# Kernel optimization log

Measured on AMD Instinct MI355X. Metric: run time of the kernel, lower is better.

## Reference

```python
import jax, jax.numpy as jnp
import numpy as np

T = 64    # target_len
D = 256   # av_dim


def setup_inputs() -> dict:
    key = jax.random.key(0)
    ks = jax.random.split(key, 8)
    B, L = 128, 512
    return {
        "acoustic_seq": jax.random.normal(ks[0], (B, L, D), jnp.float32),
        "visual_seq": jax.random.normal(ks[1], (B, L, D), jnp.float32),
        "IS_BAG_list": jnp.ones((B, L), jnp.int32),
        # h_fc: Linear(target_len, target_len)
        "Wh": jax.random.normal(ks[2], (T, T), jnp.float32) * 0.05,
        "bh": jax.random.normal(ks[3], (T,), jnp.float32) * 0.05,
        # w_fc: Linear(av_dim, av_dim)
        "Ww": jax.random.normal(ks[4], (D, D), jnp.float32) * 0.05,
        "bw": jax.random.normal(ks[5], (D,), jnp.float32) * 0.05,
        # conv: Conv2d(2, 1, kernel_size=1) -> two scalars + bias
        "conv_w": jax.random.normal(ks[6], (2,), jnp.float32) * 0.5,
        "conv_b": jax.random.normal(ks[7], (1,), jnp.float32) * 0.1,
    }


def reference(acoustic_seq, visual_seq, IS_BAG_list, Wh, bh, Ww, bw, conv_w, conv_b):
    B, L, Dd = acoustic_seq.shape
    G = L // T  # uniform group size (deterministic variant of random group sizes)
    mapping = jnp.repeat(jnp.arange(T), G)  # [L] pooled-frame index per original frame

    # resize_sequence (m_len > target_len branch): group-mean pooling to T frames
    aco_p = acoustic_seq.reshape(B, T, G, Dd).mean(axis=2)  # [B,T,D]
    vis_p = visual_seq.reshape(B, T, G, Dd).mean(axis=2)    # [B,T,D]

    # c_attention = sigmoid(Conv2d(2->1, 1x1)(stack([aco,vis], ch)))
    c_att = jax.nn.sigmoid(conv_w[0] * aco_p + conv_w[1] * vis_p + conv_b[0])  # [B,T,D]

    # hw_attention = mean over channel dim
    hw = 0.5 * (aco_p + vis_p)                                 # [B,T,D]
    h_att = jax.nn.sigmoid(hw.mean(axis=2) @ Wh.T + bh)        # [B,T]
    w_att = jax.nn.sigmoid(hw.mean(axis=1) @ Ww.T + bw)        # [B,D]

    # recover_sequence (m_len > target_len): gather attention[mapping]
    h_full = h_att[:, mapping][..., None]   # [B,L,1]
    w_full = w_att[:, None, :]              # [B,1,D]
    c_full = c_att[:, mapping, :]           # [B,L,D]

    scale = (h_full + w_full + c_full) / 3.0
    mask = (IS_BAG_list == 1)[..., None]    # [B,L,1]
    aco_out = jnp.where(mask, acoustic_seq * scale, acoustic_seq)
    vis_out = jnp.where(mask, visual_seq * scale, visual_seq)
    return aco_out, vis_out
```

## Files before the change

kernel.cpp:

```cpp
#include <hip/hip_runtime.h>
#include <math.h>

#define BB 128
#define LL 512
#define DD 256
#define TT 64
#define GG 8
#define NQ (DD/4)

typedef float f32x4 __attribute__((ext_vector_type(4)));

__device__ __forceinline__ float sigm(float x) {
    return 1.0f / (1.0f + __expf(-x));
}
__device__ __forceinline__ f32x4 sigm4(f32x4 z) {
    f32x4 r;
    r.x = sigm(z.x); r.y = sigm(z.y); r.z = sigm(z.z); r.w = sigm(z.w);
    return r;
}

__global__ __launch_bounds__(256) void k_sum(
    const f32x4* __restrict__ aco4, const f32x4* __restrict__ vis4,
    float* __restrict__ rowMean,
    float* __restrict__ colpart)
{
    const int tid  = threadIdx.x;
    const int w    = tid >> 6;
    const int lane = tid & 63;
    const int bk   = blockIdx.x;
    const int b    = bk >> 3;
    const int t8   = bk & 7;

    const size_t rowBase = (size_t)b * LL + (size_t)t8 * 64 + (size_t)w * 16;

    f32x4 hw0 = 0.f, hw1 = 0.f;
#pragma unroll
    for (int j = 0; j < 8; ++j)
        hw0 += aco4[(rowBase + j) * NQ + lane] + vis4[(rowBase + j) * NQ + lane];
#pragma unroll
    for (int j = 0; j < 8; ++j)
        hw1 += aco4[(rowBase + 8 + j) * NQ + lane] + vis4[(rowBase + 8 + j) * NQ + lane];
    hw0 *= 0.0625f;
    hw1 *= 0.0625f;

    float s0 = hw0.x + hw0.y + hw0.z + hw0.w;
    float s1 = hw1.x + hw1.y + hw1.z + hw1.w;
#pragma unroll
    for (int off = 32; off > 0; off >>= 1) {
        s0 += __shfl_xor(s0, off, 64);
        s1 += __shfl_xor(s1, off, 64);
    }
    if (lane == 0) {
        const int btBase = b * TT + t8 * 8 + 2 * w;
        rowMean[btBase]     = s0 * (1.0f / DD);
        rowMean[btBase + 1] = s1 * (1.0f / DD);
    }

    __shared__ __align__(16) float red[4][DD];
    *reinterpret_cast<f32x4*>(&red[w][lane * 4]) = hw0 + hw1;
    __syncthreads();
    colpart[(size_t)bk * DD + tid] =
        red[0][tid] + red[1][tid] + red[2][tid] + red[3][tid];
}

__global__ __launch_bounds__(256) void k_gates(
    const float* __restrict__ colpart, const float* __restrict__ rowMean,
    const float* __restrict__ Wh, const float* __restrict__ bh,
    const float* __restrict__ Ww, const float* __restrict__ bw,
    float* __restrict__ h_att, float* __restrict__ w_att)
{
    const int b = blockIdx.x;
    const int d = threadIdx.x;

    __shared__ float rm[TT];
    __shared__ float cm[DD];

    {
        float cs = 0.f;
#pragma unroll
        for (int p = 0; p < 8; ++p)
            cs += colpart[(size_t)(b * 8 + p) * DD + d];
        cm[d] = cs * (1.0f / TT);
        if (d < TT) rm[d] = rowMean[b * TT + d];
    }
    __syncthreads();

    if (d < TT) {
        float acc = bh[d];
#pragma unroll 8
        for (int j = 0; j < TT; ++j) acc += rm[j] * Wh[d * TT + j];
        h_att[b * TT + d] = sigm(acc);
    }
    {
        float acc = bw[d];
        const f32x4* Wr = reinterpret_cast<const f32x4*>(Ww + (size_t)d * DD);
#pragma unroll 8
        for (int kq = 0; kq < NQ; ++kq) {
            f32x4 wq = Wr[kq];
            acc += cm[4 * kq] * wq.x + cm[4 * kq + 1] * wq.y +
                   cm[4 * kq + 2] * wq.z + cm[4 * kq + 3] * wq.w;
        }
        w_att[b * DD + d] = sigm(acc);
    }
}

__global__ __launch_bounds__(256) void k_apply(
    const f32x4* __restrict__ aco4, const f32x4* __restrict__ vis4,
    const int* __restrict__ isb,
    const float* __restrict__ h_att, const float* __restrict__ w_att,
    const float* __restrict__ cw, const float* __restrict__ cb,
    f32x4* __restrict__ out4)
{
    const int tid = threadIdx.x;
    const int sub = tid >> 6;
    const int q   = tid & 63;
    const int bk  = blockIdx.x;
    const int b   = bk >> 4;
    const int t   = (bk & 15) * 4 + sub;

    const size_t rowBase = (size_t)b * LL + (size_t)t * GG;
    const size_t N4      = (size_t)BB * LL * NQ;

    f32x4 A[8], V[8];
#pragma unroll
    for (int j = 0; j < 8; ++j) A[j] = aco4[(rowBase + j) * NQ + q];
#pragma unroll
    for (int j = 0; j < 8; ++j) V[j] = vis4[(rowBase + j) * NQ + q];

    f32x4 pa = A[0] + A[1] + A[2] + A[3] + A[4] + A[5] + A[6] + A[7];
    f32x4 pv = V[0] + V[1] + V[2] + V[3] + V[4] + V[5] + V[6] + V[7];
    pa *= 0.125f;
    pv *= 0.125f;

    const f32x4 c  = sigm4(cw[0] * pa + cw[1] * pv + cb[0]);
    const float h  = h_att[b * TT + t];
    const f32x4 w4 = *reinterpret_cast<const f32x4*>(w_att + (size_t)b * DD + q * 4);
    const f32x4 sc = (h + w4 + c) * (1.0f / 3.0f);

#pragma unroll
    for (int j = 0; j < 8; ++j) {
        const size_t ridx = rowBase + j;
        const size_t idx  = ridx * NQ + q;
        const int m = isb[ridx];
        f32x4 a = A[j];
        f32x4 v = V[j];
        if (m == 1) { a *= sc; v *= sc; }
        __builtin_nontemporal_store(a, &out4[idx]);
        __builtin_nontemporal_store(v, &out4[N4 + idx]);
    }
}

extern "C" void kernel_launch(void* const* d_in, const int* in_sizes, int n_in,
                              void* d_out, int out_size, void* d_ws, size_t ws_size,
                              hipStream_t stream) {
    const f32x4* aco = (const f32x4*)d_in[0];
    const f32x4* vis = (const f32x4*)d_in[1];
    const int*   isb = (const int*)d_in[2];
    const float* Wh  = (const float*)d_in[3];
    const float* bh  = (const float*)d_in[4];
    const float* Ww  = (const float*)d_in[5];
    const float* bw  = (const float*)d_in[6];
    const float* cw  = (const float*)d_in[7];
    const float* cb  = (const float*)d_in[8];
    f32x4* out = (f32x4*)d_out;

    float* ws = (float*)d_ws;
    float* rowMean = ws;
    float* colpart = rowMean + BB * TT;
    float* h_att   = colpart + 1024 * DD;
    float* w_att   = h_att + BB * TT;

    k_sum<<<1024, 256, 0, stream>>>(aco, vis, rowMean, colpart);
    k_gates<<<BB, 256, 0, stream>>>(colpart, rowMean, Wh, bh, Ww, bw, h_att, w_att);
    k_apply<<<2048, 256, 0, stream>>>(aco, vis, isb, h_att, w_att, cw, cb, out);
}
```

Before: 77.21 us.

## Fuse gate computation into apply kernel, recomputing gates per block

```diff
diff --git a/kernel.cpp b/kernel.cpp
--- a/kernel.cpp
+++ b/kernel.cpp
@@ -63,51 +63,12 @@
         red[0][tid] + red[1][tid] + red[2][tid] + red[3][tid];
 }
 
-__global__ __launch_bounds__(256) void k_gates(
+__global__ __launch_bounds__(256) void k_apply(
+    const f32x4* __restrict__ aco4, const f32x4* __restrict__ vis4,
+    const int* __restrict__ isb,
     const float* __restrict__ colpart, const float* __restrict__ rowMean,
     const float* __restrict__ Wh, const float* __restrict__ bh,
     const float* __restrict__ Ww, const float* __restrict__ bw,
-    float* __restrict__ h_att, float* __restrict__ w_att)
-{
-    const int b = blockIdx.x;
-    const int d = threadIdx.x;
-
-    __shared__ float rm[TT];
-    __shared__ float cm[DD];
-
-    {
-        float cs = 0.f;
-#pragma unroll
-        for (int p = 0; p < 8; ++p)
-            cs += colpart[(size_t)(b * 8 + p) * DD + d];
-        cm[d] = cs * (1.0f / TT);
-        if (d < TT) rm[d] = rowMean[b * TT + d];
-    }
-    __syncthreads();
-
-    if (d < TT) {
-        float acc = bh[d];
-#pragma unroll 8
-        for (int j = 0; j < TT; ++j) acc += rm[j] * Wh[d * TT + j];
-        h_att[b * TT + d] = sigm(acc);
-    }
-    {
-        float acc = bw[d];
-        const f32x4* Wr = reinterpret_cast<const f32x4*>(Ww + (size_t)d * DD);
-#pragma unroll 8
-        for (int kq = 0; kq < NQ; ++kq) {
-            f32x4 wq = Wr[kq];
-            acc += cm[4 * kq] * wq.x + cm[4 * kq + 1] * wq.y +
-                   cm[4 * kq + 2] * wq.z + cm[4 * kq + 3] * wq.w;
-        }
-        w_att[b * DD + d] = sigm(acc);
-    }
-}
-
-__global__ __launch_bounds__(256) void k_apply(
-    const f32x4* __restrict__ aco4, const f32x4* __restrict__ vis4,
-    const int* __restrict__ isb,
-    const float* __restrict__ h_att, const float* __restrict__ w_att,
     const float* __restrict__ cw, const float* __restrict__ cb,
     f32x4* __restrict__ out4)
 {
@@ -127,14 +88,49 @@
 #pragma unroll
     for (int j = 0; j < 8; ++j) V[j] = vis4[(rowBase + j) * NQ + q];
 
+    __shared__ __align__(16) float cm[DD];
+    __shared__ __align__(16) float w_l[DD];
+    __shared__ float rm[TT];
+    __shared__ float h_l[4];
+
+    {
+        float cs = 0.f;
+#pragma unroll
+        for (int p = 0; p < 8; ++p)
+            cs += colpart[(size_t)(b * 8 + p) * DD + tid];
+        cm[tid] = cs * (1.0f / TT);
+        if (tid < TT) rm[tid] = rowMean[b * TT + tid];
+    }
+    __syncthreads();
+
+    if (tid < 4) {
+        const int tt = (bk & 15) * 4 + tid;
+        float acc = bh[tt];
+#pragma unroll 8
+        for (int j = 0; j < TT; ++j) acc += rm[j] * Wh[tt * TT + j];
+        h_l[tid] = sigm(acc);
+    }
+    {
+        float acc = bw[tid];
+        const f32x4* Wr = reinterpret_cast<const f32x4*>(Ww + (size_t)tid * DD);
+#pragma unroll 8
+        for (int kq = 0; kq < NQ; ++kq) {
+            f32x4 wq = Wr[kq];
+            acc += cm[4 * kq] * wq.x + cm[4 * kq + 1] * wq.y +
+                   cm[4 * kq + 2] * wq.z + cm[4 * kq + 3] * wq.w;
+        }
+        w_l[tid] = sigm(acc);
+    }
+    __syncthreads();
+
     f32x4 pa = A[0] + A[1] + A[2] + A[3] + A[4] + A[5] + A[6] + A[7];
     f32x4 pv = V[0] + V[1] + V[2] + V[3] + V[4] + V[5] + V[6] + V[7];
     pa *= 0.125f;
     pv *= 0.125f;
 
     const f32x4 c  = sigm4(cw[0] * pa + cw[1] * pv + cb[0]);
-    const float h  = h_att[b * TT + t];
-    const f32x4 w4 = *reinterpret_cast<const f32x4*>(w_att + (size_t)b * DD + q * 4);
+    const float h  = h_l[sub];
+    const f32x4 w4 = *reinterpret_cast<const f32x4*>(&w_l[q * 4]);
     const f32x4 sc = (h + w4 + c) * (1.0f / 3.0f);
 
 #pragma unroll
@@ -167,10 +163,8 @@
     float* ws = (float*)d_ws;
     float* rowMean = ws;
     float* colpart = rowMean + BB * TT;
-    float* h_att   = colpart + 1024 * DD;
-    float* w_att   = h_att + BB * TT;
 
     k_sum<<<1024, 256, 0, stream>>>(aco, vis, rowMean, colpart);
-    k_gates<<<BB, 256, 0, stream>>>(colpart, rowMean, Wh, bh, Ww, bw, h_att, w_att);
-    k_apply<<<2048, 256, 0, stream>>>(aco, vis, isb, h_att, w_att, cw, cb, out);
+    k_apply<<<2048, 256, 0, stream>>>(aco, vis, isb, colpart, rowMean,
+                                      Wh, bh, Ww, bw, cw, cb, out);
 }
```

New measurement: 104.4 us. 1.35x slower.
